# Performance work log

Hardware: AMD Instinct MI355X
Metric: run time of the kernel (lower is better)

The kernel has to match this reference:

```python
import jax, jax.numpy as jnp
import numpy as np

N, E, D_IN, D_H, D_OUT, N_LAYERS = 100000, 1600000, 128, 128, 40, 2


def setup_inputs() -> dict:
    key = jax.random.key(0)
    ks = jax.random.split(key, 10)
    s = 1.0 / np.sqrt(D_H)
    inp = {
        "x": jax.random.normal(ks[0], (N, D_IN), dtype=jnp.float32),
        "edge_index": jax.random.randint(ks[1], (2, E), 0, N, dtype=jnp.int64),
        "W_embed": jax.random.uniform(ks[2], (D_IN, D_H), jnp.float32, -s, s),
        "b_embed": jnp.zeros((D_H,), jnp.float32),
        "W_conv1": jax.random.uniform(ks[3], (D_H, D_H), jnp.float32, -s, s),
        "b_conv1": jnp.zeros((D_H,), jnp.float32),
        "W_conv2": jax.random.uniform(ks[4], (D_H, D_H), jnp.float32, -s, s),
        "b_conv2": jnp.zeros((D_H,), jnp.float32),
        "W_cls": jax.random.uniform(ks[5], (D_H * (N_LAYERS + 1), D_OUT), jnp.float32, -s, s),
        "b_cls": jnp.zeros((D_OUT,), jnp.float32),
    }
    return inp


def _gcn_conv(h, W, b, src, dst, dinv):
    # PyG GCNConv: h' = D^{-1/2} (A+I) D^{-1/2} (h W) + b  (self-loops already in src/dst)
    h = h @ W                                   # [N, D]
    norm = dinv[src] * dinv[dst]                # [E+N]
    msg = h[src] * norm[:, None]                # [E+N, D]  gather + scale
    return jax.ops.segment_sum(msg, dst, num_segments=N) + b


def reference(x, edge_index, W_embed, b_embed, W_conv1, b_conv1, W_conv2, b_conv2, W_cls, b_cls):
    loops = jnp.arange(N, dtype=edge_index.dtype)
    src = jnp.concatenate([edge_index[0], loops])
    dst = jnp.concatenate([edge_index[1], loops])
    deg = jnp.zeros((N,), jnp.float32).at[dst].add(1.0)   # in-degree incl. self-loop (>=1)
    dinv = jax.lax.rsqrt(deg)

    # dropout is identity in eval mode (training=False)
    h = jax.nn.relu(x @ W_embed + b_embed)
    reps = [h]
    for W, b in ((W_conv1, b_conv1), (W_conv2, b_conv2)):
        h = jax.nn.relu(_gcn_conv(h, W, b, src, dst, dinv))
        reps.append(h)
    return jnp.concatenate(reps, axis=-1) @ W_cls + b_cls
```

## Files before the change

### kernel.cpp

```cpp
#include <hip/hip_runtime.h>

constexpr int Nn   = 100000;
constexpr int Ee   = 1600000;
constexpr int D    = 128;
constexpr int DOUT = 40;
constexpr int DCAT = 384;
constexpr int CPAD = 48;
constexpr int WS   = 392;

constexpr int BINSH  = 8;
constexpr int BINSZ  = 1 << BINSH;
constexpr int BINS   = (Nn + BINSZ - 1) / BINSZ;
constexpr int CHUNK  = 8192;
constexpr int NCHUNK = (Ee + CHUNK - 1) / CHUNK;
constexpr int SEGCAP = 5376;
constexpr int PADCAP = SEGCAP + 7 * BINSZ;

typedef _Float16 f16;
typedef _Float16 f16x2 __attribute__((ext_vector_type(2)));
typedef _Float16 f16x4 __attribute__((ext_vector_type(4)));
typedef _Float16 f16x8 __attribute__((ext_vector_type(8)));
typedef float    f32x2 __attribute__((ext_vector_type(2)));
typedef float    f32x4 __attribute__((ext_vector_type(4)));
typedef int      i32x4 __attribute__((ext_vector_type(4)));

__device__ inline int detect_flag(const int* __restrict__ ei) {
    unsigned orv = 0;
#pragma unroll
    for (int j = 1; j < 16; j += 2) orv |= (unsigned)ei[j];
    return orv == 0u;
}

__device__ inline void load_edge(const int* __restrict__ ei, int f, int e, int& s, int& d) {
    if (f) {
        s = ((const int2*)ei)[e].x;
        d = ((const int2*)ei)[Ee + e].x;
    } else {
        s = ei[e];
        d = ei[Ee + e];
    }
}

__device__ inline int* scan_incl(int* pa, int* pb, int n2, int tid) {
    for (int off = 1; off < n2; off <<= 1) {
        for (int i = tid; i < n2; i += 256) pb[i] = pa[i] + ((i >= off) ? pa[i - off] : 0);
        __syncthreads();
        int* t = pa; pa = pb; pb = t;
    }
    return pa;
}

__global__ __launch_bounds__(256) void bin_scatter(const int* __restrict__ ei,
                                                   int* __restrict__ binCursor,
                                                   unsigned* __restrict__ arena) {
    __shared__ unsigned srec[CHUNK];
    __shared__ int bcnt[BINS], bpfx[BINS], bfill[BINS], gbase[BINS];
    __shared__ int pA[512], pB[512];
    const int tid = threadIdx.x;
    const int e0 = blockIdx.x * CHUNK;
    const int n = min(CHUNK, Ee - e0);
    const int f = detect_flag(ei);

    for (int i = tid; i < BINS; i += 256) { bcnt[i] = 0; bfill[i] = 0; }
    __syncthreads();
    for (int i = tid; i < n; i += 256) {
        int s, d;
        load_edge(ei, f, e0 + i, s, d);
        if ((unsigned)s < (unsigned)Nn && (unsigned)d < (unsigned)Nn)
            atomicAdd(&bcnt[d >> BINSH], 1);
    }
    __syncthreads();
    for (int i = tid; i < 512; i += 256) pA[i] = (i < BINS) ? bcnt[i] : 0;
    __syncthreads();
    int* incl = scan_incl(pA, pB, 512, tid);
    for (int i = tid; i < BINS; i += 256) {
        bpfx[i] = incl[i] - bcnt[i];
        gbase[i] = bcnt[i] ? atomicAdd(&binCursor[i], bcnt[i]) : 0;
    }
    __syncthreads();
    for (int i = tid; i < n; i += 256) {
        int s, d;
        load_edge(ei, f, e0 + i, s, d);
        if ((unsigned)s < (unsigned)Nn && (unsigned)d < (unsigned)Nn) {
            int bin = d >> BINSH;
            int lp = atomicAdd(&bfill[bin], 1);
            srec[bpfx[bin] + lp] = ((unsigned)(d & (BINSZ - 1)) << 17) | (unsigned)s;
        }
    }
    __syncthreads();
    const int wid = tid >> 6, lane = tid & 63;
    for (int bin = wid; bin < BINS; bin += 4) {
        int cnt = bcnt[bin], off = bpfx[bin], gb = gbase[bin];
        for (int j = lane; j < cnt; j += 64)
            if (gb + j < SEGCAP) arena[(size_t)bin * SEGCAP + gb + j] = srec[off + j];
    }
}

__global__ __launch_bounds__(256) void bin_finalize(const int* __restrict__ binCursor,
                                                    const unsigned* __restrict__ arena,
                                                    float* __restrict__ dinv,
                                                    int* __restrict__ sortedSrc,
                                                    i32x4* __restrict__ rec) {
    __shared__ unsigned seg[SEGCAP];
    __shared__ int ssrc[PADCAP];
    __shared__ int cnt[BINSZ], fill[BINSZ], pA[BINSZ], pB[BINSZ];
    const int tid = threadIdx.x;
    const int b = blockIdx.x;
    int len = binCursor[b];
    if (len > SEGCAP) len = SEGCAP;

    for (int i = tid; i < len; i += 256) seg[i] = arena[(size_t)b * SEGCAP + i];
    for (int i = tid; i < BINSZ; i += 256) { cnt[i] = 0; fill[i] = 0; }
    __syncthreads();
    for (int i = tid; i < len; i += 256) atomicAdd(&cnt[seg[i] >> 17], 1);
    __syncthreads();
    for (int i = tid; i < BINSZ; i += 256) pA[i] = (cnt[i] + 7) & ~7;
    __syncthreads();
    int* incl = scan_incl(pA, pB, BINSZ, tid);

    const int node0 = b * BINSZ;
    const int padLen = incl[BINSZ - 1];
    for (int i = tid; i < padLen; i += 256) ssrc[i] = Nn;
    __syncthreads();
    for (int i = tid; i < len; i += 256) {
        unsigned r = seg[i];
        int dl = r >> 17, s = (int)(r & 0x1FFFFu);
        int pc = (cnt[dl] + 7) & ~7;
        int p = atomicAdd(&fill[dl], 1);
        ssrc[incl[dl] - pc + p] = s;
    }
    __syncthreads();
    for (int t = tid; t < BINSZ; t += 256) {
        int node = node0 + t;
        if (node < Nn) {
            int c = cnt[t];
            int pc = (c + 7) & ~7;
            int start = incl[t] - pc;
            float dv = rsqrtf((float)(c + 1));
            dinv[node] = dv;
            i32x4 r0, r1, r2;
#pragma unroll
            for (int j = 0; j < 4; ++j) r0[j] = (j < pc) ? ssrc[start + j] : Nn;
#pragma unroll
            for (int j = 0; j < 4; ++j) r1[j] = (4 + j < pc) ? ssrc[start + 4 + j] : Nn;
            r2[0] = b * PADCAP + start;
            r2[1] = c;
            r2[2] = __float_as_int(dv);
            r2[3] = 0;
            rec[(size_t)node * 3 + 0] = r0;
            rec[(size_t)node * 3 + 1] = r1;
            rec[(size_t)node * 3 + 2] = r2;
        }
    }
    __syncthreads();
    for (int i = tid; i < padLen; i += 256) sortedSrc[(size_t)b * PADCAP + i] = ssrc[i];
}

__global__ __launch_bounds__(256) void prep_all(const float* __restrict__ W0,
                                                const float* __restrict__ W1,
                                                const float* __restrict__ W2,
                                                const float* __restrict__ Wc,
                                                f16* __restrict__ WtAll,
                                                f16* __restrict__ Wct,
                                                unsigned char* __restrict__ tmp8) {
    int b = blockIdx.x;
    if (b < 3) {
        const float* W = (b == 0) ? W0 : ((b == 1) ? W1 : W2);
        f16* Wt = WtAll + (size_t)b * D * D;
        for (int i = threadIdx.x; i < D * D; i += 256) {
            int k = i >> 7, c = i & 127;
            Wt[c * D + k] = (f16)W[i];
        }
    } else {
        if (threadIdx.x < 32)
            ((unsigned*)(tmp8 + (size_t)Nn * 128))[threadIdx.x] = 0u;
        for (int i = threadIdx.x; i < CPAD * WS; i += 256) {
            int c = i / WS, k = i - c * WS;
            f16 v = (f16)0.0f;
            if (c < DOUT && k < DCAT) v = (f16)Wc[k * DOUT + c];
            Wct[i] = v;
        }
    }
}

__global__ __launch_bounds__(256) void gemm_fused01(const float* __restrict__ x,
                                                    const f16* __restrict__ WeT,
                                                    const f16* __restrict__ W1T,
                                                    const float* __restrict__ b_embed,
                                                    const float* __restrict__ dinv,
                                                    f16* __restrict__ hcat,
                                                    unsigned char* __restrict__ tmp8) {
    __shared__ f16 Bsw[128 * 128];
    __shared__ f16 Hsw[128 * 128];
    const int tid = threadIdx.x;
    const int r0 = blockIdx.x * 128;
    const int lane = tid & 63;
    const int w = tid >> 6;
    const int wr = w * 32;

    {
        int row = tid >> 1, half = (tid & 1) * 128;
#pragma unroll
        for (int i = 0; i < 8; ++i) {
            int bir = half + i * 16;
            uint4 v = *(const uint4*)((const char*)WeT + (size_t)row * 256 + bir);
            *(uint4*)((char*)Bsw + row * 256 + (bir ^ ((row & 7) << 4))) = v;
        }
    }
    __syncthreads();

    f32x4 acc[2][8];
#pragma unroll
    for (int mf = 0; mf < 2; ++mf)
#pragma unroll
        for (int nf = 0; nf < 8; ++nf) acc[mf][nf] = (f32x4){0, 0, 0, 0};

#pragma unroll
    for (int kk = 0; kk < 4; ++kk) {
        const int ke = kk * 32 + (lane >> 4) * 8;
        f16x8 a[2], b[8];
#pragma unroll
        for (int mf = 0; mf < 2; ++mf) {
            int row = r0 + wr + mf * 16 + (lane & 15);
            int rc = (row < Nn) ? row : (Nn - 1);
            const float* p = x + (size_t)rc * D + ke;
            float4 f0 = *(const float4*)p;
            float4 f1 = *(const float4*)(p + 4);
            f16x8 h;
            h[0] = (f16)f0.x; h[1] = (f16)f0.y; h[2] = (f16)f0.z; h[3] = (f16)f0.w;
            h[4] = (f16)f1.x; h[5] = (f16)f1.y; h[6] = (f16)f1.z; h[7] = (f16)f1.w;
            a[mf] = h;
        }
#pragma unroll
        for (int nf = 0; nf < 8; ++nf) {
            int col = nf * 16 + (lane & 15);
            int bir = kk * 64 + (lane >> 4) * 16;
            b[nf] = *(const f16x8*)((const char*)Bsw + col * 256 + (bir ^ ((col & 7) << 4)));
        }
#pragma unroll
        for (int mf = 0; mf < 2; ++mf)
#pragma unroll
            for (int nf = 0; nf < 8; ++nf)
                acc[mf][nf] = __builtin_amdgcn_mfma_f32_16x16x32_f16(a[mf], b[nf], acc[mf][nf], 0, 0, 0);
    }

    {
        float bv[8];
#pragma unroll
        for (int nf = 0; nf < 8; ++nf) bv[nf] = b_embed[nf * 16 + (lane & 15)];
#pragma unroll
        for (int mf = 0; mf < 2; ++mf) {
#pragma unroll
            for (int i = 0; i < 4; ++i) {
                int lrow = wr + mf * 16 + (lane >> 4) * 4 + i;
                int row = r0 + lrow;
#pragma unroll
                for (int nf = 0; nf < 8; ++nf) {
                    float v = acc[mf][nf][i] + bv[nf];
                    if (v < 0.0f) v = 0.0f;
                    f16 hv = (f16)v;
                    if (row < Nn) hcat[(size_t)row * DCAT + nf * 16 + (lane & 15)] = hv;
                    int bir = (nf * 16 + (lane & 15)) * 2;
                    *(f16*)((char*)Hsw + lrow * 256 + (bir ^ ((lrow & 7) << 4))) = hv;
                }
            }
        }
    }
    __syncthreads();

    {
        int row = tid >> 1, half = (tid & 1) * 128;
#pragma unroll
        for (int i = 0; i < 8; ++i) {
            int bir = half + i * 16;
            uint4 v = *(const uint4*)((const char*)W1T + (size_t)row * 256 + bir);
            *(uint4*)((char*)Bsw + row * 256 + (bir ^ ((row & 7) << 4))) = v;
        }
    }
#pragma unroll
    for (int mf = 0; mf < 2; ++mf)
#pragma unroll
        for (int nf = 0; nf < 8; ++nf) acc[mf][nf] = (f32x4){0, 0, 0, 0};
    __syncthreads();

#pragma unroll
    for (int kk = 0; kk < 4; ++kk) {
        f16x8 a[2], b[8];
#pragma unroll
        for (int mf = 0; mf < 2; ++mf) {
            int lrow = wr + mf * 16 + (lane & 15);
            int bir = kk * 64 + (lane >> 4) * 16;
            a[mf] = *(const f16x8*)((const char*)Hsw + lrow * 256 + (bir ^ ((lrow & 7) << 4)));
        }
#pragma unroll
        for (int nf = 0; nf < 8; ++nf) {
            int col = nf * 16 + (lane & 15);
            int bir = kk * 64 + (lane >> 4) * 16;
            b[nf] = *(const f16x8*)((const char*)Bsw + col * 256 + (bir ^ ((col & 7) << 4)));
        }
#pragma unroll
        for (int mf = 0; mf < 2; ++mf)
#pragma unroll
            for (int nf = 0; nf < 8; ++nf)
                acc[mf][nf] = __builtin_amdgcn_mfma_f32_16x16x32_f16(a[mf], b[nf], acc[mf][nf], 0, 0, 0);
    }

#pragma unroll
    for (int mf = 0; mf < 2; ++mf) {
#pragma unroll
        for (int i = 0; i < 4; ++i) {
            int row = r0 + wr + mf * 16 + (lane >> 4) * 4 + i;
            if (row < Nn) {
                float sc = dinv[row];
#pragma unroll
                for (int nf = 0; nf < 8; ++nf) {
                    float v = acc[mf][nf][i] * sc;
                    unsigned pk = __builtin_amdgcn_cvt_pk_fp8_f32(v, v, 0, false);
                    tmp8[(size_t)row * 128 + nf * 16 + (lane & 15)] = (unsigned char)pk;
                }
            }
        }
    }
}

__global__ __launch_bounds__(256) void gemm_mfma(const f16* __restrict__ Ain, int sA,
                                                 const f16* __restrict__ Wt,
                                                 const float* __restrict__ scale,
                                                 unsigned char* __restrict__ tmp8,
                                                 int M) {
    __shared__ f16 Bsw[128 * 128];
    const int tid = threadIdx.x;
    const int r0 = blockIdx.x * 128;

    {
        int row = tid >> 1, half = (tid & 1) * 128;
#pragma unroll
        for (int i = 0; i < 8; ++i) {
            int bir = half + i * 16;
            uint4 v = *(const uint4*)((const char*)Wt + (size_t)row * 256 + bir);
            *(uint4*)((char*)Bsw + row * 256 + (bir ^ ((row & 7) << 4))) = v;
        }
    }
    __syncthreads();

    const int lane = tid & 63;
    const int w    = tid >> 6;
    const int wr   = w * 32;

    f32x4 acc[2][8];
#pragma unroll
    for (int mf = 0; mf < 2; ++mf)
#pragma unroll
        for (int nf = 0; nf < 8; ++nf) acc[mf][nf] = (f32x4){0, 0, 0, 0};

#pragma unroll
    for (int kk = 0; kk < 4; ++kk) {
        const int ke = kk * 32 + (lane >> 4) * 8;
        f16x8 a[2], b[8];
#pragma unroll
        for (int mf = 0; mf < 2; ++mf) {
            int row = r0 + wr + mf * 16 + (lane & 15);
            int rc = (row < M) ? row : (M - 1);
            a[mf] = *(const f16x8*)(Ain + (size_t)rc * sA + ke);
        }
#pragma unroll
        for (int nf = 0; nf < 8; ++nf) {
            int col = nf * 16 + (lane & 15);
            int bir = kk * 64 + (lane >> 4) * 16;
            b[nf] = *(const f16x8*)((const char*)Bsw + col * 256 + (bir ^ ((col & 7) << 4)));
        }
#pragma unroll
        for (int mf = 0; mf < 2; ++mf)
#pragma unroll
            for (int nf = 0; nf < 8; ++nf)
                acc[mf][nf] = __builtin_amdgcn_mfma_f32_16x16x32_f16(a[mf], b[nf], acc[mf][nf], 0, 0, 0);
    }

#pragma unroll
    for (int mf = 0; mf < 2; ++mf) {
#pragma unroll
        for (int i = 0; i < 4; ++i) {
            int row = r0 + wr + mf * 16 + (lane >> 4) * 4 + i;
            if (row < M) {
                float sc = scale[row];
#pragma unroll
                for (int nf = 0; nf < 8; ++nf) {
                    float v = acc[mf][nf][i] * sc;
                    unsigned pk = __builtin_amdgcn_cvt_pk_fp8_f32(v, v, 0, false);
                    tmp8[(size_t)row * 128 + nf * 16 + (lane & 15)] = (unsigned char)pk;
                }
            }
        }
    }
}

__global__ __launch_bounds__(256) void aggregate_pad(const unsigned char* __restrict__ tmp8,
                                                     const i32x4* __restrict__ rec,
                                                     const int* __restrict__ sortedSrc,
                                                     const float* __restrict__ bias,
                                                     f16* __restrict__ hcat, int partOff) {
    int node = (blockIdx.x * 256 + threadIdx.x) >> 6;
    int lane = threadIdx.x & 63;
    int l32  = lane & 31;
    int h    = lane >> 5;
    if (node >= Nn) return;
    const unsigned* t4 = (const unsigned*)tmp8;

    i32x4 rI = rec[(size_t)node * 3 + h];
    i32x4 rM = rec[(size_t)node * 3 + 2];
    unsigned sv = t4[(size_t)node * 32 + l32];

    int base = rM[0];
    int pc = (rM[1] + 7) & ~7;
    float di = __int_as_float(rM[2]);

    f32x2 aLo = (f32x2){0.0f, 0.0f};
    f32x2 aHi = (f32x2){0.0f, 0.0f};
    if (h == 0) {
        aLo = __builtin_amdgcn_cvt_pk_f32_fp8((int)sv, false);
        aHi = __builtin_amdgcn_cvt_pk_f32_fp8((int)sv, true);
    }

    {
        unsigned g0 = t4[(size_t)rI[0] * 32 + l32];
        unsigned g1 = t4[(size_t)rI[1] * 32 + l32];
        unsigned g2 = t4[(size_t)rI[2] * 32 + l32];
        unsigned g3 = t4[(size_t)rI[3] * 32 + l32];
        aLo += __builtin_amdgcn_cvt_pk_f32_fp8((int)g0, false);
        aHi += __builtin_amdgcn_cvt_pk_f32_fp8((int)g0, true);
        aLo += __builtin_amdgcn_cvt_pk_f32_fp8((int)g1, false);
        aHi += __builtin_amdgcn_cvt_pk_f32_fp8((int)g1, true);
        aLo += __builtin_amdgcn_cvt_pk_f32_fp8((int)g2, false);
        aHi += __builtin_amdgcn_cvt_pk_f32_fp8((int)g2, true);
        aLo += __builtin_amdgcn_cvt_pk_f32_fp8((int)g3, false);
        aHi += __builtin_amdgcn_cvt_pk_f32_fp8((int)g3, true);
    }

    for (int e = 8; e < pc; e += 8) {
        i32x4 idx = *(const i32x4*)(sortedSrc + base + e + h * 4);
        unsigned g0 = t4[(size_t)idx[0] * 32 + l32];
        unsigned g1 = t4[(size_t)idx[1] * 32 + l32];
        unsigned g2 = t4[(size_t)idx[2] * 32 + l32];
        unsigned g3 = t4[(size_t)idx[3] * 32 + l32];
        aLo += __builtin_amdgcn_cvt_pk_f32_fp8((int)g0, false);
        aHi += __builtin_amdgcn_cvt_pk_f32_fp8((int)g0, true);
        aLo += __builtin_amdgcn_cvt_pk_f32_fp8((int)g1, false);
        aHi += __builtin_amdgcn_cvt_pk_f32_fp8((int)g1, true);
        aLo += __builtin_amdgcn_cvt_pk_f32_fp8((int)g2, false);
        aHi += __builtin_amdgcn_cvt_pk_f32_fp8((int)g2, true);
        aLo += __builtin_amdgcn_cvt_pk_f32_fp8((int)g3, false);
        aHi += __builtin_amdgcn_cvt_pk_f32_fp8((int)g3, true);
    }

    aLo[0] += __shfl_xor(aLo[0], 32);
    aLo[1] += __shfl_xor(aLo[1], 32);
    aHi[0] += __shfl_xor(aHi[0], 32);
    aHi[1] += __shfl_xor(aHi[1], 32);

    if (h == 0) {
        float4 bb = *(const float4*)(bias + l32 * 4);
        float o0 = di * aLo[0] + bb.x;
        float o1 = di * aLo[1] + bb.y;
        float o2 = di * aHi[0] + bb.z;
        float o3 = di * aHi[1] + bb.w;
        if (o0 < 0.0f) o0 = 0.0f;
        if (o1 < 0.0f) o1 = 0.0f;
        if (o2 < 0.0f) o2 = 0.0f;
        if (o3 < 0.0f) o3 = 0.0f;
        f16x4 o;
        o[0] = (f16)o0; o[1] = (f16)o1; o[2] = (f16)o2; o[3] = (f16)o3;
        *(f16x4*)(hcat + (size_t)node * DCAT + partOff + l32 * 4) = o;
    }
}

__global__ __launch_bounds__(256) void cls_mfma(const f16* __restrict__ hcat,
                                                const f16* __restrict__ Wct,
                                                const float* __restrict__ bc,
                                                float* __restrict__ out) {
    __shared__ f16 Bs[CPAD * WS];
    const int tid = threadIdx.x;
    for (int i = tid; i < CPAD * WS / 8; i += 256)
        ((uint4*)Bs)[i] = ((const uint4*)Wct)[i];
    __syncthreads();

    const int lane = tid & 63;
    const int w    = tid >> 6;
    const int r0   = blockIdx.x * 128 + w * 32;

    f32x4 acc[2][3];
#pragma unroll
    for (int mf = 0; mf < 2; ++mf)
#pragma unroll
        for (int nf = 0; nf < 3; ++nf) acc[mf][nf] = (f32x4){0, 0, 0, 0};

#pragma unroll 3
    for (int kk = 0; kk < 12; ++kk) {
        const int ke = kk * 32 + (lane >> 4) * 8;
        f16x8 a[2], b[3];
#pragma unroll
        for (int mf = 0; mf < 2; ++mf) {
            int row = r0 + mf * 16 + (lane & 15);
            int rc = (row < Nn) ? row : (Nn - 1);
            a[mf] = *(const f16x8*)(hcat + (size_t)rc * DCAT + ke);
        }
#pragma unroll
        for (int nf = 0; nf < 3; ++nf) {
            int col = nf * 16 + (lane & 15);
            b[nf] = *(const f16x8*)(Bs + col * WS + ke);
        }
#pragma unroll
        for (int mf = 0; mf < 2; ++mf)
#pragma unroll
            for (int nf = 0; nf < 3; ++nf)
                acc[mf][nf] = __builtin_amdgcn_mfma_f32_16x16x32_f16(a[mf], b[nf], acc[mf][nf], 0, 0, 0);
    }

    float bv[3];
#pragma unroll
    for (int nf = 0; nf < 3; ++nf) {
        int col = nf * 16 + (lane & 15);
        bv[nf] = (col < DOUT) ? bc[col] : 0.0f;
    }
#pragma unroll
    for (int mf = 0; mf < 2; ++mf) {
#pragma unroll
        for (int i = 0; i < 4; ++i) {
            int row = r0 + mf * 16 + (lane >> 4) * 4 + i;
            if (row < Nn) {
#pragma unroll
                for (int nf = 0; nf < 3; ++nf) {
                    int col = nf * 16 + (lane & 15);
                    if (col < DOUT) out[(size_t)row * DOUT + col] = acc[mf][nf][i] + bv[nf];
                }
            }
        }
    }
}

extern "C" void kernel_launch(void* const* d_in, const int* in_sizes, int n_in,
                              void* d_out, int out_size, void* d_ws, size_t ws_size,
                              hipStream_t stream) {
    const float* x       = (const float*)d_in[0];
    const int*   ei      = (const int*)d_in[1];
    const float* W_embed = (const float*)d_in[2];
    const float* b_embed = (const float*)d_in[3];
    const float* W_conv1 = (const float*)d_in[4];
    const float* b_conv1 = (const float*)d_in[5];
    const float* W_conv2 = (const float*)d_in[6];
    const float* b_conv2 = (const float*)d_in[7];
    const float* W_cls   = (const float*)d_in[8];
    const float* b_cls   = (const float*)d_in[9];
    float* out = (float*)d_out;

    char* p = (char*)d_ws;
    size_t o = 0;
    auto carve = [&](size_t bytes) {
        char* r = p + o;
        o = (o + bytes + 255) & ~(size_t)255;
        return r;
    };
    int*      binCursor = (int*)carve((size_t)BINS * 4);
    int*      sortedSrc = (int*)carve(((size_t)BINS * PADCAP + 1024) * 4);
    i32x4*    rec       = (i32x4*)carve((size_t)Nn * 48);
    float*    dinv      = (float*)carve((size_t)Nn * 4);
    f16*      WtAll     = (f16*)carve((size_t)3 * D * D * 2);
    f16*      Wct       = (f16*)carve((size_t)CPAD * WS * 2);
    f16*      hcat      = (f16*)carve((size_t)Nn * DCAT * 2);
    unsigned char* tmp8 = (unsigned char*)carve((size_t)(Nn + 1) * 128);
    (void)ws_size;

    unsigned* arena = (unsigned*)hcat;

    hipMemsetAsync(binCursor, 0, (size_t)BINS * 4, stream);
    bin_scatter<<<NCHUNK, 256, 0, stream>>>(ei, binCursor, arena);
    bin_finalize<<<BINS, 256, 0, stream>>>(binCursor, arena, dinv, sortedSrc, rec);
    prep_all<<<4, 256, 0, stream>>>(W_embed, W_conv1, W_conv2, W_cls, WtAll, Wct, tmp8);

    const int gGemm = (Nn + 127) / 128;
    const int gAgg  = (Nn * 64) / 256;

    gemm_fused01<<<gGemm, 256, 0, stream>>>(x, WtAll, WtAll + D * D, b_embed, dinv, hcat, tmp8);
    aggregate_pad<<<gAgg, 256, 0, stream>>>(tmp8, rec, sortedSrc, b_conv1, hcat, D);
    gemm_mfma<<<gGemm, 256, 0, stream>>>(hcat + D, DCAT, WtAll + 2 * D * D, dinv, tmp8, Nn);
    aggregate_pad<<<gAgg, 256, 0, stream>>>(tmp8, rec, sortedSrc, b_conv2, hcat, 2 * D);
    cls_mfma<<<gGemm, 256, 0, stream>>>(hcat, Wct, b_cls, out);
}
```

Baseline: 236.9 us.

## Replace two-level binned CSR build with global-atomic counting sort

Replaces the shared-memory bin scatter and per-bin finalize with a direct counting sort: global degree atomics, a per-bin scan that sets row bases, an atomic placement pass, and a small rec_build kernel. This removes the arena staging through hcat and the large per-block shared-memory usage that limited occupancy. In exchange it relies on scattered global atomics across 100k counters and adds more kernel launches. Edge order within a row becomes nondeterministic, and invalid sources are now kept as padding entries rather than dropped.

```diff
diff --git a/kernel.cpp b/kernel.cpp
--- a/kernel.cpp
+++ b/kernel.cpp
@@ -11,8 +11,6 @@
 constexpr int BINSH  = 8;
 constexpr int BINSZ  = 1 << BINSH;
 constexpr int BINS   = (Nn + BINSZ - 1) / BINSZ;
-constexpr int CHUNK  = 8192;
-constexpr int NCHUNK = (Ee + CHUNK - 1) / CHUNK;
 constexpr int SEGCAP = 5376;
 constexpr int PADCAP = SEGCAP + 7 * BINSZ;
 
@@ -41,119 +39,83 @@
     }
 }
 
-__device__ inline int* scan_incl(int* pa, int* pb, int n2, int tid) {
-    for (int off = 1; off < n2; off <<= 1) {
-        for (int i = tid; i < n2; i += 256) pb[i] = pa[i] + ((i >= off) ? pa[i - off] : 0);
+__global__ __launch_bounds__(256) void deg_count(const int* __restrict__ ei,
+                                                 int* __restrict__ deg) {
+    int f = detect_flag(ei);
+    for (int e = blockIdx.x * 256 + threadIdx.x; e < Ee; e += gridDim.x * 256) {
+        int d = f ? ((const int2*)ei)[Ee + e].x : ei[Ee + e];
+        if ((unsigned)d < (unsigned)Nn) atomicAdd(&deg[d], 1);
+    }
+}
+
+__global__ __launch_bounds__(256) void node_scan(const int* __restrict__ deg,
+                                                 int* __restrict__ rowBase,
+                                                 float* __restrict__ dinv,
+                                                 i32x4* __restrict__ rec,
+                                                 int* __restrict__ sortedSrc) {
+    __shared__ int a[256], b2[256];
+    const int t = threadIdx.x;
+    const int b = blockIdx.x;
+    const int node = b * BINSZ + t;
+    int c = (node < Nn) ? deg[node] : 0;
+    int pc = (c + 7) & ~7;
+    int* pa = a;
+    int* pb = b2;
+    pa[t] = pc;
+    __syncthreads();
+    for (int off = 1; off < 256; off <<= 1) {
+        int v = pa[t] + ((t >= off) ? pa[t - off] : 0);
         __syncthreads();
-        int* t = pa; pa = pb; pb = t;
-    }
-    return pa;
-}
-
-__global__ __launch_bounds__(256) void bin_scatter(const int* __restrict__ ei,
-                                                   int* __restrict__ binCursor,
-                                                   unsigned* __restrict__ arena) {
-    __shared__ unsigned srec[CHUNK];
-    __shared__ int bcnt[BINS], bpfx[BINS], bfill[BINS], gbase[BINS];
-    __shared__ int pA[512], pB[512];
-    const int tid = threadIdx.x;
-    const int e0 = blockIdx.x * CHUNK;
-    const int n = min(CHUNK, Ee - e0);
-    const int f = detect_flag(ei);
-
-    for (int i = tid; i < BINS; i += 256) { bcnt[i] = 0; bfill[i] = 0; }
-    __syncthreads();
-    for (int i = tid; i < n; i += 256) {
+        pb[t] = v;
+        __syncthreads();
+        int* tmp = pa; pa = pb; pb = tmp;
+    }
+    int base = b * PADCAP + pa[t] - pc;
+    if (node < Nn) {
+        rowBase[node] = base;
+        float dv = rsqrtf((float)(c + 1));
+        dinv[node] = dv;
+        i32x4 r2;
+        r2[0] = base;
+        r2[1] = c;
+        r2[2] = __float_as_int(dv);
+        r2[3] = 0;
+        rec[(size_t)node * 3 + 2] = r2;
+        for (int j = c; j < pc; ++j) sortedSrc[base + j] = Nn;
+    }
+}
+
+__global__ __launch_bounds__(256) void place(const int* __restrict__ ei,
+                                             const int* __restrict__ rowBase,
+                                             int* __restrict__ fill,
+                                             int* __restrict__ sortedSrc) {
+    int f = detect_flag(ei);
+    for (int e = blockIdx.x * 256 + threadIdx.x; e < Ee; e += gridDim.x * 256) {
         int s, d;
-        load_edge(ei, f, e0 + i, s, d);
-        if ((unsigned)s < (unsigned)Nn && (unsigned)d < (unsigned)Nn)
-            atomicAdd(&bcnt[d >> BINSH], 1);
-    }
-    __syncthreads();
-    for (int i = tid; i < 512; i += 256) pA[i] = (i < BINS) ? bcnt[i] : 0;
-    __syncthreads();
-    int* incl = scan_incl(pA, pB, 512, tid);
-    for (int i = tid; i < BINS; i += 256) {
-        bpfx[i] = incl[i] - bcnt[i];
-        gbase[i] = bcnt[i] ? atomicAdd(&binCursor[i], bcnt[i]) : 0;
-    }
-    __syncthreads();
-    for (int i = tid; i < n; i += 256) {
-        int s, d;
-        load_edge(ei, f, e0 + i, s, d);
-        if ((unsigned)s < (unsigned)Nn && (unsigned)d < (unsigned)Nn) {
-            int bin = d >> BINSH;
-            int lp = atomicAdd(&bfill[bin], 1);
-            srec[bpfx[bin] + lp] = ((unsigned)(d & (BINSZ - 1)) << 17) | (unsigned)s;
-        }
-    }
-    __syncthreads();
-    const int wid = tid >> 6, lane = tid & 63;
-    for (int bin = wid; bin < BINS; bin += 4) {
-        int cnt = bcnt[bin], off = bpfx[bin], gb = gbase[bin];
-        for (int j = lane; j < cnt; j += 64)
-            if (gb + j < SEGCAP) arena[(size_t)bin * SEGCAP + gb + j] = srec[off + j];
-    }
-}
-
-__global__ __launch_bounds__(256) void bin_finalize(const int* __restrict__ binCursor,
-                                                    const unsigned* __restrict__ arena,
-                                                    float* __restrict__ dinv,
-                                                    int* __restrict__ sortedSrc,
-                                                    i32x4* __restrict__ rec) {
-    __shared__ unsigned seg[SEGCAP];
-    __shared__ int ssrc[PADCAP];
-    __shared__ int cnt[BINSZ], fill[BINSZ], pA[BINSZ], pB[BINSZ];
-    const int tid = threadIdx.x;
-    const int b = blockIdx.x;
-    int len = binCursor[b];
-    if (len > SEGCAP) len = SEGCAP;
-
-    for (int i = tid; i < len; i += 256) seg[i] = arena[(size_t)b * SEGCAP + i];
-    for (int i = tid; i < BINSZ; i += 256) { cnt[i] = 0; fill[i] = 0; }
-    __syncthreads();
-    for (int i = tid; i < len; i += 256) atomicAdd(&cnt[seg[i] >> 17], 1);
-    __syncthreads();
-    for (int i = tid; i < BINSZ; i += 256) pA[i] = (cnt[i] + 7) & ~7;
-    __syncthreads();
-    int* incl = scan_incl(pA, pB, BINSZ, tid);
-
-    const int node0 = b * BINSZ;
-    const int padLen = incl[BINSZ - 1];
-    for (int i = tid; i < padLen; i += 256) ssrc[i] = Nn;
-    __syncthreads();
-    for (int i = tid; i < len; i += 256) {
-        unsigned r = seg[i];
-        int dl = r >> 17, s = (int)(r & 0x1FFFFu);
-        int pc = (cnt[dl] + 7) & ~7;
-        int p = atomicAdd(&fill[dl], 1);
-        ssrc[incl[dl] - pc + p] = s;
-    }
-    __syncthreads();
-    for (int t = tid; t < BINSZ; t += 256) {
-        int node = node0 + t;
-        if (node < Nn) {
-            int c = cnt[t];
-            int pc = (c + 7) & ~7;
-            int start = incl[t] - pc;
-            float dv = rsqrtf((float)(c + 1));
-            dinv[node] = dv;
-            i32x4 r0, r1, r2;
-#pragma unroll
-            for (int j = 0; j < 4; ++j) r0[j] = (j < pc) ? ssrc[start + j] : Nn;
-#pragma unroll
-            for (int j = 0; j < 4; ++j) r1[j] = (4 + j < pc) ? ssrc[start + 4 + j] : Nn;
-            r2[0] = b * PADCAP + start;
-            r2[1] = c;
-            r2[2] = __float_as_int(dv);
-            r2[3] = 0;
-            rec[(size_t)node * 3 + 0] = r0;
-            rec[(size_t)node * 3 + 1] = r1;
-            rec[(size_t)node * 3 + 2] = r2;
-        }
-    }
-    __syncthreads();
-    for (int i = tid; i < padLen; i += 256) sortedSrc[(size_t)b * PADCAP + i] = ssrc[i];
+        load_edge(ei, f, e, s, d);
+        if ((unsigned)d < (unsigned)Nn) {
+            int ss = ((unsigned)s < (unsigned)Nn) ? s : Nn;
+            int slot = atomicAdd(&fill[d], 1);
+            sortedSrc[rowBase[d] + slot] = ss;
+        }
+    }
+}
+
+__global__ __launch_bounds__(256) void rec_build(const int* __restrict__ rowBase,
+                                                 const int* __restrict__ deg,
+                                                 int* __restrict__ sortedSrc,
+                                                 i32x4* __restrict__ rec) {
+    int node = blockIdx.x * 256 + threadIdx.x;
+    if (node >= Nn) return;
+    int base = rowBase[node];
+    int pc = (deg[node] + 7) & ~7;
+    i32x4 r0, r1;
+#pragma unroll
+    for (int j = 0; j < 4; ++j) r0[j] = (j < pc) ? sortedSrc[base + j] : Nn;
+#pragma unroll
+    for (int j = 0; j < 4; ++j) r1[j] = (4 + j < pc) ? sortedSrc[base + 4 + j] : Nn;
+    rec[(size_t)node * 3 + 0] = r0;
+    rec[(size_t)node * 3 + 1] = r1;
 }
 
 __global__ __launch_bounds__(256) void prep_all(const float* __restrict__ W0,
@@ -559,7 +521,9 @@
         o = (o + bytes + 255) & ~(size_t)255;
         return r;
     };
-    int*      binCursor = (int*)carve((size_t)BINS * 4);
+    int*      deg       = (int*)carve((size_t)2 * Nn * 4);
+    int*      fill      = deg + Nn;
+    int*      rowBase   = (int*)carve((size_t)Nn * 4);
     int*      sortedSrc = (int*)carve(((size_t)BINS * PADCAP + 1024) * 4);
     i32x4*    rec       = (i32x4*)carve((size_t)Nn * 48);
     float*    dinv      = (float*)carve((size_t)Nn * 4);
@@ -569,11 +533,11 @@
     unsigned char* tmp8 = (unsigned char*)carve((size_t)(Nn + 1) * 128);
     (void)ws_size;
 
-    unsigned* arena = (unsigned*)hcat;
-
-    hipMemsetAsync(binCursor, 0, (size_t)BINS * 4, stream);
-    bin_scatter<<<NCHUNK, 256, 0, stream>>>(ei, binCursor, arena);
-    bin_finalize<<<BINS, 256, 0, stream>>>(binCursor, arena, dinv, sortedSrc, rec);
+    hipMemsetAsync(deg, 0, (size_t)2 * Nn * 4, stream);
+    deg_count<<<1024, 256, 0, stream>>>(ei, deg);
+    node_scan<<<BINS, 256, 0, stream>>>(deg, rowBase, dinv, rec, sortedSrc);
+    place<<<2048, 256, 0, stream>>>(ei, rowBase, fill, sortedSrc);
+    rec_build<<<(Nn + 255) / 256, 256, 0, stream>>>(rowBase, deg, sortedSrc, rec);
     prep_all<<<4, 256, 0, stream>>>(W_embed, W_conv1, W_conv2, W_cls, WtAll, Wct, tmp8);
 
     const int gGemm = (Nn + 127) / 128;
```

New measurement: 362.7 us. 53.1% more time.
